# Kernel optimization log

Hardware: AMD Instinct MI355X
Metric: run time of the kernel (lower is better)

## Reference

```python
import jax, jax.numpy as jnp
import numpy as np

EMBED_DIM = 1024
NUM_HEADS = 16
HEAD_DIM = EMBED_DIM // NUM_HEADS
B, N = 4, 2048


def setup_inputs() -> dict:
    key = jax.random.key(0)
    k = jax.random.split(key, 5)
    s = 1.0 / np.sqrt(EMBED_DIM)
    return {
        "x": jax.random.normal(k[0], (B, N, EMBED_DIM), dtype=jnp.float32),
        "W_qkv": jax.random.uniform(k[1], (EMBED_DIM, 3 * EMBED_DIM), jnp.float32, -s, s),
        "b_qkv": jax.random.uniform(k[2], (3 * EMBED_DIM,), jnp.float32, -s, s),
        "W_proj": jax.random.uniform(k[3], (EMBED_DIM, EMBED_DIM), jnp.float32, -s, s),
        "b_proj": jax.random.uniform(k[4], (EMBED_DIM,), jnp.float32, -s, s),
    }


def reference(x, W_qkv, b_qkv, W_proj, b_proj):
    b, n, c = x.shape
    qkv = x @ W_qkv + b_qkv                       # [B,N,3C]
    qkv = qkv.reshape(b, n, 3, NUM_HEADS, HEAD_DIM)
    q = qkv[:, :, 0].transpose(0, 2, 1, 3)        # [B,H,N,D]
    k = qkv[:, :, 1].transpose(0, 2, 1, 3)
    v = qkv[:, :, 2].transpose(0, 2, 1, 3)
    scale = 1.0 / np.sqrt(HEAD_DIM).astype(np.float32)
    scores = jnp.einsum("bhqd,bhkd->bhqk", q, k) * scale
    attn = jax.nn.softmax(scores, axis=-1)
    out = jnp.einsum("bhqk,bhkd->bhqd", attn, v)  # [B,H,N,D]
    out = out.transpose(0, 2, 1, 3).reshape(b, n, c)
    return out @ W_proj + b_proj
```

## Files before the change

kernel.cpp:

```cpp
#include <hip/hip_runtime.h>
#include <math.h>


typedef __bf16 bf16x8 __attribute__((ext_vector_type(8)));
typedef float f32x4 __attribute__((ext_vector_type(4)));

#define EMBED 1024
#define NHEAD 16
#define BATCH 4
#define SEQ 2048
#define M_TOT 8192
#define QKV_N 3072
#define QSCALE 0.18033688011112042f

__device__ __forceinline__ ushort f2bf(float f) {
  union { float f; unsigned u; } x; x.f = f;
  unsigned r = x.u + 0x7FFFu + ((x.u >> 16) & 1u);
  return (ushort)(r >> 16);
}

__device__ __forceinline__ uint cvt2bf(float a, float b) {
#if __has_builtin(__builtin_amdgcn_cvt_pk_bf16_f32)
  typedef __bf16 bf16x2 __attribute__((ext_vector_type(2)));
  union { bf16x2 v; uint u; } c;
  c.v = __builtin_amdgcn_cvt_pk_bf16_f32(a, b);
  return c.u;
#else
  return (uint)f2bf(a) | ((uint)f2bf(b) << 16);
#endif
}

__device__ __forceinline__ float fexp2(float x) {
#if __has_builtin(__builtin_amdgcn_exp2f)
  return __builtin_amdgcn_exp2f(x);
#else
  return exp2f(x);
#endif
}

__device__ __forceinline__ f32x4 mfma16(bf16x8 a, bf16x8 b, f32x4 c) {
  return __builtin_amdgcn_mfma_f32_16x16x32_bf16(a, b, c, 0, 0, 0);
}

__device__ __forceinline__ void gl2lds16(const void* g, void* l) {
  __builtin_amdgcn_global_load_lds(
      (const __attribute__((address_space(1))) unsigned int*)g,
      (__attribute__((address_space(3))) unsigned int*)l, 16, 0, 0);
}

__global__ __launch_bounds__(256) void cvt_f32_bf16(
    const float* __restrict__ in, ushort* __restrict__ out) {
  int i = (blockIdx.x * 256 + threadIdx.x) * 4;
  float4 v = *reinterpret_cast<const float4*>(&in[i]);
  uint2 w = {cvt2bf(v.x, v.y), cvt2bf(v.z, v.w)};
  *reinterpret_cast<uint2*>(&out[i]) = w;
}

__global__ __launch_bounds__(256) void transpose_to_bf16(
    const float* __restrict__ in, ushort* __restrict__ out, int Kd, int Nd) {
  __shared__ float tile[64][65];
  const int t = threadIdx.x;
  const int n0 = blockIdx.x * 64, k0 = blockIdx.y * 64;
#pragma unroll
  for (int i = 0; i < 16; ++i) {
    int e = t + 256 * i;
    int kr = e >> 6, nc = e & 63;
    tile[kr][nc] = in[(size_t)(k0 + kr) * Nd + n0 + nc];
  }
  __syncthreads();
#pragma unroll
  for (int i = 0; i < 16; ++i) {
    int e = t + 256 * i;
    int nr = e >> 6, kc = e & 63;
    out[(size_t)(n0 + nr) * Kd + k0 + kc] = f2bf(tile[kc][nr]);
  }
}

__global__ __launch_bounds__(256) void gemm_bf16(
    const ushort* __restrict__ A, const ushort* __restrict__ Bt,
    const float* __restrict__ bias, void* __restrict__ Cout,
    ushort* __restrict__ vtgout, int M, int N, int K, int mode) {
  __shared__ ushort As[128 * 32];
  __shared__ ushort Bs[128 * 32];
  const int t = threadIdx.x;
  const int wave = t >> 6, lane = t & 63;
  const int lane15 = lane & 15, quad = lane >> 4;
  const int m0 = blockIdx.y * 128, n0 = blockIdx.x * 128;
  const int wm = (wave >> 1) * 64, wn = (wave & 1) * 64;

  int srow[2], scol[2], sdst[2];
#pragma unroll
  for (int j = 0; j < 2; ++j) {
    int c = (j * 4 + wave) * 64 + lane;
    int row = c >> 2;
    scol[j] = (((c & 3) ^ ((row >> 1) & 3)) * 8);
    srow[j] = row;
    sdst[j] = (j * 4 + wave) * 512;
  }
  const int swG = (lane15 >> 1) & 3;

  f32x4 acc[4][4] = {};

  for (int k0 = 0; k0 < K; k0 += 32) {
#pragma unroll
    for (int j = 0; j < 2; ++j) {
      gl2lds16(&A[(size_t)(m0 + srow[j]) * K + k0 + scol[j]], &As[sdst[j]]);
      gl2lds16(&Bt[(size_t)(n0 + srow[j]) * K + k0 + scol[j]], &Bs[sdst[j]]);
    }
    __syncthreads();

    bf16x8 af[4], bfr[4];
#pragma unroll
    for (int ms = 0; ms < 4; ++ms)
      af[ms] = *reinterpret_cast<const bf16x8*>(
          &As[(wm + ms * 16 + lane15) * 32 + ((quad ^ swG) * 8)]);
#pragma unroll
    for (int ns = 0; ns < 4; ++ns)
      bfr[ns] = *reinterpret_cast<const bf16x8*>(
          &Bs[(wn + ns * 16 + lane15) * 32 + ((quad ^ swG) * 8)]);
#pragma unroll
    for (int ms = 0; ms < 4; ++ms)
#pragma unroll
      for (int ns = 0; ns < 4; ++ns)
        acc[ms][ns] = mfma16(af[ms], bfr[ns], acc[ms][ns]);
    __syncthreads();
  }

  if (mode == 0) {
    float* out = (float*)Cout;
#pragma unroll
    for (int ns = 0; ns < 4; ++ns) {
      int col = n0 + wn + ns * 16 + lane15;
      float bv = bias[col];
#pragma unroll
      for (int ms = 0; ms < 4; ++ms)
#pragma unroll
        for (int r = 0; r < 4; ++r) {
          int row = m0 + wm + ms * 16 + quad * 4 + r;
          out[(size_t)row * N + col] = acc[ms][ns][r] + bv;
        }
    }
  } else {
    ushort* qk = (ushort*)Cout;
#pragma unroll
    for (int ns = 0; ns < 4; ++ns) {
      int col = n0 + wn + ns * 16 + lane15;
      float bv = bias[col];
      if (col < 2048) {
        float sc = (col < 1024) ? QSCALE : 1.0f;
#pragma unroll
        for (int ms = 0; ms < 4; ++ms) {
          int row = m0 + wm + ms * 16 + quad * 4;
          uint u01 = cvt2bf((acc[ms][ns][0] + bv) * sc, (acc[ms][ns][1] + bv) * sc);
          uint u23 = cvt2bf((acc[ms][ns][2] + bv) * sc, (acc[ms][ns][3] + bv) * sc);
          qk[(size_t)(row + 0) * 2048 + col] = (ushort)u01;
          qk[(size_t)(row + 1) * 2048 + col] = (ushort)(u01 >> 16);
          qk[(size_t)(row + 2) * 2048 + col] = (ushort)u23;
          qk[(size_t)(row + 3) * 2048 + col] = (ushort)(u23 >> 16);
        }
      } else {
        int dp = col - 2048;
#pragma unroll
        for (int ms = 0; ms < 4; ++ms) {
          int row = m0 + wm + ms * 16 + quad * 4;
          int b = row >> 11, seq = row & 2047;
          uint2 w = {cvt2bf(acc[ms][ns][0] + bv, acc[ms][ns][1] + bv),
                     cvt2bf(acc[ms][ns][2] + bv, acc[ms][ns][3] + bv)};
          *reinterpret_cast<uint2*>(
              &vtgout[((size_t)(b * 1024 + dp) << 11) + seq]) = w;
        }
      }
    }
  }
}

#define QG 2

__global__ __launch_bounds__(256, 4) void attn_kernel(
    const ushort* __restrict__ qk, const ushort* __restrict__ vtg,
    ushort* __restrict__ out) {
  __shared__ ushort Ks[2][4096];
  __shared__ ushort Vt[2][4096];
  __shared__ ushort Ps[4][16 * 64];

  const int t = threadIdx.x;
  const int wave = t >> 6, lane = t & 63;
  const int lane15 = lane & 15, quad = lane >> 4;
  const int bh = blockIdx.x, qg = blockIdx.y;
  const int b = bh >> 4, h = bh & 15;
  const size_t boff = (size_t)b * SEQ * 2048;

  int sdst[2];
  const ushort* kptr[2];
  const ushort* vptr[2];
#pragma unroll
  for (int j = 0; j < 2; ++j) {
    int lg = (j * 4 + wave) * 64 + lane;
    int row = lg >> 3;
    int col = ((lg & 7) ^ (row & 7)) * 8;
    sdst[j] = (j * 4 + wave) * 512;
    kptr[j] = qk + boff + (size_t)row * 2048 + 1024 + h * 64 + col;
    vptr[j] = vtg + ((size_t)(b * 1024 + h * 64 + row) << 11) + col;
  }

  bf16x8 qf[QG][2];
#pragma unroll
  for (int g = 0; g < QG; ++g) {
    size_t qoff = boff +
        (size_t)(qg * (QG * 64) + g * 64 + wave * 16 + lane15) * 2048 + h * 64;
    qf[g][0] = *reinterpret_cast<const bf16x8*>(&qk[qoff + quad * 8]);
    qf[g][1] = *reinterpret_cast<const bf16x8*>(&qk[qoff + 32 + quad * 8]);
  }

  bf16x8 ones;
#pragma unroll
  for (int j = 0; j < 8; ++j) ones[j] = (__bf16)1.0f;

  f32x4 O[QG][4] = {};
  f32x4 lacc[QG] = {};
  const int sw = lane15 & 7;
  ushort* ps = Ps[wave];

#pragma unroll
  for (int j = 0; j < 2; ++j) {
    gl2lds16(kptr[j], &Ks[0][sdst[j]]);
    gl2lds16(vptr[j], &Vt[0][sdst[j]]);
  }
  __syncthreads();

  for (int kt = 0; kt < SEQ / 64; ++kt) {
    const int cur = kt & 1, nxt = cur ^ 1;
    if (kt < SEQ / 64 - 1) {
#pragma unroll
      for (int j = 0; j < 2; ++j) {
        gl2lds16(kptr[j] + (size_t)(kt + 1) * 64 * 2048, &Ks[nxt][sdst[j]]);
        gl2lds16(vptr[j] + (kt + 1) * 64, &Vt[nxt][sdst[j]]);
      }
    }

    bf16x8 kf[4][2];
#pragma unroll
    for (int nsub = 0; nsub < 4; ++nsub) {
      const int kr = (nsub * 16 + lane15) * 64;
      kf[nsub][0] = *reinterpret_cast<const bf16x8*>(
          &Ks[cur][kr + ((quad ^ sw) * 8)]);
      kf[nsub][1] = *reinterpret_cast<const bf16x8*>(
          &Ks[cur][kr + (((quad + 4) ^ sw) * 8)]);
    }

#pragma unroll
    for (int g = 0; g < QG; ++g) {
      f32x4 st[4];
#pragma unroll
      for (int nsub = 0; nsub < 4; ++nsub) {
        f32x4 a = {-32.0f, -32.0f, -32.0f, -32.0f};
        a = mfma16(kf[nsub][0], qf[g][0], a);
        a = mfma16(kf[nsub][1], qf[g][1], a);
        st[nsub] = a;
      }
#pragma unroll
      for (int nsub = 0; nsub < 4; ++nsub) {
        uint2 w = {cvt2bf(fexp2(st[nsub][0]), fexp2(st[nsub][1])),
                   cvt2bf(fexp2(st[nsub][2]), fexp2(st[nsub][3]))};
        *reinterpret_cast<uint2*>(
            &ps[lane15 * 64 + (((2 * nsub + (quad >> 1)) ^ sw) << 3) +
                ((quad & 1) << 2)]) = w;
      }
#pragma unroll
      for (int kk = 0; kk < 2; ++kk) {
        bf16x8 pf = *reinterpret_cast<const bf16x8*>(
            &ps[lane15 * 64 + (((kk * 4 + quad) ^ sw) << 3)]);
#pragma unroll
        for (int dsub = 0; dsub < 4; ++dsub) {
          int d = dsub * 16 + lane15;
          bf16x8 vf = *reinterpret_cast<const bf16x8*>(
              &Vt[cur][d * 64 + (((kk * 4 + quad) ^ sw) * 8)]);
          O[g][dsub] = mfma16(pf, vf, O[g][dsub]);
        }
        lacc[g] = mfma16(pf, ones, lacc[g]);
      }
    }
    __syncthreads();
  }

#pragma unroll
  for (int g = 0; g < QG; ++g)
#pragma unroll
    for (int r = 0; r < 4; ++r) {
      float linv = __builtin_amdgcn_rcpf(lacc[g][r]);
      size_t rowoff =
          (size_t)(b * SEQ + qg * (QG * 64) + g * 64 + wave * 16 + quad * 4 +
                   r) * EMBED + h * 64;
      uint u01 = cvt2bf(O[g][0][r] * linv, O[g][1][r] * linv);
      uint u23 = cvt2bf(O[g][2][r] * linv, O[g][3][r] * linv);
      out[rowoff + 0 * 16 + lane15] = (ushort)u01;
      out[rowoff + 1 * 16 + lane15] = (ushort)(u01 >> 16);
      out[rowoff + 2 * 16 + lane15] = (ushort)u23;
      out[rowoff + 3 * 16 + lane15] = (ushort)(u23 >> 16);
    }
}

extern "C" void kernel_launch(void* const* d_in, const int* in_sizes, int n_in,
                              void* d_out, int out_size, void* d_ws,
                              size_t ws_size, hipStream_t stream) {
  const float* x = (const float*)d_in[0];
  const float* Wqkv = (const float*)d_in[1];
  const float* bqkv = (const float*)d_in[2];
  const float* Wproj = (const float*)d_in[3];
  const float* bproj = (const float*)d_in[4];
  float* out = (float*)d_out;

  char* ws = (char*)d_ws;
  ushort* Wqkv_t = (ushort*)ws;
  ushort* Wproj_t = (ushort*)(ws + 6291456);
  ushort* qk = (ushort*)(ws + 8388608);
  ushort* vtg = (ushort*)(ws + 41943040);
  ushort* xb = (ushort*)(ws + 58720256);
  ushort* attnout = (ushort*)(ws + 58720256);

  cvt_f32_bf16<<<M_TOT * EMBED / 1024, 256, 0, stream>>>(x, xb);
  transpose_to_bf16<<<dim3(QKV_N / 64, EMBED / 64), 256, 0, stream>>>(
      Wqkv, Wqkv_t, EMBED, QKV_N);
  transpose_to_bf16<<<dim3(EMBED / 64, EMBED / 64), 256, 0, stream>>>(
      Wproj, Wproj_t, EMBED, EMBED);
  gemm_bf16<<<dim3(QKV_N / 128, M_TOT / 128), 256, 0, stream>>>(
      xb, Wqkv_t, bqkv, qk, vtg, M_TOT, QKV_N, EMBED, 1);
  attn_kernel<<<dim3(NHEAD * BATCH, SEQ / (QG * 64)), 256, 0, stream>>>(
      qk, vtg, attnout);
  gemm_bf16<<<dim3(EMBED / 128, M_TOT / 128), 256, 0, stream>>>(
      attnout, Wproj_t, bproj, out, nullptr, M_TOT, EMBED, EMBED, 0);
}
```

Before: 310.5 us.

## Fuse prep kernels, deepen GEMM K-tile to 64, hoist V fragment loads

Merges the x conversion and both weight transposes into one launch with block-index dispatch, removing two kernel launches. The GEMM K tile grows from 32 to 64 with an 8-way XOR swizzle, which halves the barrier and loop overhead per K and doubles shared memory per block. The attention kernel loads V fragments once per key tile instead of once per query group, which reduces LDS reads at the cost of more registers.

```diff
diff --git a/kernel.cpp b/kernel.cpp
--- a/kernel.cpp
+++ b/kernel.cpp
@@ -48,19 +48,32 @@
       (__attribute__((address_space(3))) unsigned int*)l, 16, 0, 0);
 }
 
-__global__ __launch_bounds__(256) void cvt_f32_bf16(
-    const float* __restrict__ in, ushort* __restrict__ out) {
-  int i = (blockIdx.x * 256 + threadIdx.x) * 4;
-  float4 v = *reinterpret_cast<const float4*>(&in[i]);
-  uint2 w = {cvt2bf(v.x, v.y), cvt2bf(v.z, v.w)};
-  *reinterpret_cast<uint2*>(&out[i]) = w;
-}
-
-__global__ __launch_bounds__(256) void transpose_to_bf16(
-    const float* __restrict__ in, ushort* __restrict__ out, int Kd, int Nd) {
+__global__ __launch_bounds__(256) void prep_kernel(
+    const float* __restrict__ x, ushort* __restrict__ xb,
+    const float* __restrict__ Wqkv, ushort* __restrict__ Wqkv_t,
+    const float* __restrict__ Wproj, ushort* __restrict__ Wproj_t) {
   __shared__ float tile[64][65];
+  const int bid = blockIdx.x;
   const int t = threadIdx.x;
-  const int n0 = blockIdx.x * 64, k0 = blockIdx.y * 64;
+  if (bid < 8192) {
+    int i = (bid * 256 + t) * 4;
+    float4 v = *reinterpret_cast<const float4*>(&x[i]);
+    uint2 w = {cvt2bf(v.x, v.y), cvt2bf(v.z, v.w)};
+    *reinterpret_cast<uint2*>(&xb[i]) = w;
+    return;
+  }
+  const float* in;
+  ushort* out;
+  int Kd = 1024, Nd, n0, k0;
+  if (bid < 8960) {
+    int b2 = bid - 8192;
+    in = Wqkv; out = Wqkv_t; Nd = 3072;
+    n0 = (b2 % 48) * 64; k0 = (b2 / 48) * 64;
+  } else {
+    int b2 = bid - 8960;
+    in = Wproj; out = Wproj_t; Nd = 1024;
+    n0 = (b2 % 16) * 64; k0 = (b2 / 16) * 64;
+  }
 #pragma unroll
   for (int i = 0; i < 16; ++i) {
     int e = t + 256 * i;
@@ -80,49 +93,52 @@
     const ushort* __restrict__ A, const ushort* __restrict__ Bt,
     const float* __restrict__ bias, void* __restrict__ Cout,
     ushort* __restrict__ vtgout, int M, int N, int K, int mode) {
-  __shared__ ushort As[128 * 32];
-  __shared__ ushort Bs[128 * 32];
+  __shared__ ushort As[128 * 64];
+  __shared__ ushort Bs[128 * 64];
   const int t = threadIdx.x;
   const int wave = t >> 6, lane = t & 63;
   const int lane15 = lane & 15, quad = lane >> 4;
   const int m0 = blockIdx.y * 128, n0 = blockIdx.x * 128;
   const int wm = (wave >> 1) * 64, wn = (wave & 1) * 64;
 
-  int srow[2], scol[2], sdst[2];
-#pragma unroll
-  for (int j = 0; j < 2; ++j) {
+  int srow[4], scol[4], sdst[4];
+#pragma unroll
+  for (int j = 0; j < 4; ++j) {
     int c = (j * 4 + wave) * 64 + lane;
-    int row = c >> 2;
-    scol[j] = (((c & 3) ^ ((row >> 1) & 3)) * 8);
+    int row = c >> 3;
+    scol[j] = ((c & 7) ^ (row & 7)) * 8;
     srow[j] = row;
     sdst[j] = (j * 4 + wave) * 512;
   }
-  const int swG = (lane15 >> 1) & 3;
+  const int sw = lane15 & 7;
 
   f32x4 acc[4][4] = {};
 
-  for (int k0 = 0; k0 < K; k0 += 32) {
-#pragma unroll
-    for (int j = 0; j < 2; ++j) {
+  for (int k0 = 0; k0 < K; k0 += 64) {
+#pragma unroll
+    for (int j = 0; j < 4; ++j) {
       gl2lds16(&A[(size_t)(m0 + srow[j]) * K + k0 + scol[j]], &As[sdst[j]]);
       gl2lds16(&Bt[(size_t)(n0 + srow[j]) * K + k0 + scol[j]], &Bs[sdst[j]]);
     }
     __syncthreads();
 
-    bf16x8 af[4], bfr[4];
-#pragma unroll
-    for (int ms = 0; ms < 4; ++ms)
-      af[ms] = *reinterpret_cast<const bf16x8*>(
-          &As[(wm + ms * 16 + lane15) * 32 + ((quad ^ swG) * 8)]);
-#pragma unroll
-    for (int ns = 0; ns < 4; ++ns)
-      bfr[ns] = *reinterpret_cast<const bf16x8*>(
-          &Bs[(wn + ns * 16 + lane15) * 32 + ((quad ^ swG) * 8)]);
-#pragma unroll
-    for (int ms = 0; ms < 4; ++ms)
+#pragma unroll
+    for (int kk = 0; kk < 2; ++kk) {
+      bf16x8 af[4], bfr[4];
+#pragma unroll
+      for (int ms = 0; ms < 4; ++ms)
+        af[ms] = *reinterpret_cast<const bf16x8*>(
+            &As[(wm + ms * 16 + lane15) * 64 + (((kk * 4 + quad) ^ sw) * 8)]);
 #pragma unroll
       for (int ns = 0; ns < 4; ++ns)
-        acc[ms][ns] = mfma16(af[ms], bfr[ns], acc[ms][ns]);
+        bfr[ns] = *reinterpret_cast<const bf16x8*>(
+            &Bs[(wn + ns * 16 + lane15) * 64 + (((kk * 4 + quad) ^ sw) * 8)]);
+#pragma unroll
+      for (int ms = 0; ms < 4; ++ms)
+#pragma unroll
+        for (int ns = 0; ns < 4; ++ns)
+          acc[ms][ns] = mfma16(af[ms], bfr[ns], acc[ms][ns]);
+    }
     __syncthreads();
   }
 
@@ -238,7 +254,7 @@
       }
     }
 
-    bf16x8 kf[4][2];
+    bf16x8 kf[4][2], vf[2][4];
 #pragma unroll
     for (int nsub = 0; nsub < 4; ++nsub) {
       const int kr = (nsub * 16 + lane15) * 64;
@@ -247,6 +263,14 @@
       kf[nsub][1] = *reinterpret_cast<const bf16x8*>(
           &Ks[cur][kr + (((quad + 4) ^ sw) * 8)]);
     }
+#pragma unroll
+    for (int kk = 0; kk < 2; ++kk)
+#pragma unroll
+      for (int dsub = 0; dsub < 4; ++dsub) {
+        int d = dsub * 16 + lane15;
+        vf[kk][dsub] = *reinterpret_cast<const bf16x8*>(
+            &Vt[cur][d * 64 + (((kk * 4 + quad) ^ sw) * 8)]);
+      }
 
 #pragma unroll
     for (int g = 0; g < QG; ++g) {
@@ -271,12 +295,8 @@
         bf16x8 pf = *reinterpret_cast<const bf16x8*>(
             &ps[lane15 * 64 + (((kk * 4 + quad) ^ sw) << 3)]);
 #pragma unroll
-        for (int dsub = 0; dsub < 4; ++dsub) {
-          int d = dsub * 16 + lane15;
-          bf16x8 vf = *reinterpret_cast<const bf16x8*>(
-              &Vt[cur][d * 64 + (((kk * 4 + quad) ^ sw) * 8)]);
-          O[g][dsub] = mfma16(pf, vf, O[g][dsub]);
-        }
+        for (int dsub = 0; dsub < 4; ++dsub)
+          O[g][dsub] = mfma16(pf, vf[kk][dsub], O[g][dsub]);
         lacc[g] = mfma16(pf, ones, lacc[g]);
       }
     }
@@ -318,11 +338,8 @@
   ushort* xb = (ushort*)(ws + 58720256);
   ushort* attnout = (ushort*)(ws + 58720256);
 
-  cvt_f32_bf16<<<M_TOT * EMBED / 1024, 256, 0, stream>>>(x, xb);
-  transpose_to_bf16<<<dim3(QKV_N / 64, EMBED / 64), 256, 0, stream>>>(
-      Wqkv, Wqkv_t, EMBED, QKV_N);
-  transpose_to_bf16<<<dim3(EMBED / 64, EMBED / 64), 256, 0, stream>>>(
-      Wproj, Wproj_t, EMBED, EMBED);
+  prep_kernel<<<8192 + 768 + 256, 256, 0, stream>>>(
+      x, xb, Wqkv, Wqkv_t, Wproj, Wproj_t);
   gemm_bf16<<<dim3(QKV_N / 128, M_TOT / 128), 256, 0, stream>>>(
       xb, Wqkv_t, bqkv, qk, vtg, M_TOT, QKV_N, EMBED, 1);
   attn_kernel<<<dim3(NHEAD * BATCH, SEQ / (QG * 64)), 256, 0, stream>>>(
```

New measurement: 290.2 us. 6.5% less time.
